# Kernel tuning notes

Measured on AMD Instinct MI355X. Metric: run time of the kernel, lower is better.

The kernel has to match this reference:

```python
import jax, jax.numpy as jnp
import numpy as np

B, S, D, H, O = 8, 4096, 512, 512, 512
NS, NC, SD = 4, 4, 8
CLIP, TEMP, SUP_SCALE, SUP_EPS, LN_EPS = 3.0, 1.0, 1.0, 1e-4, 1e-5


def _ln(x, w, b):
    m = jnp.mean(x, -1, keepdims=True)
    v = jnp.mean((x - m) ** 2, -1, keepdims=True)
    return (x - m) * jax.lax.rsqrt(v + LN_EPS) * w + b


def _lin(x, w, b):
    return x @ w.T + b


def setup_inputs() -> dict:
    key = jax.random.key(0)
    ks = iter(jax.random.split(key, 32))

    def W(shape):
        return 0.02 * jax.random.normal(next(ks), shape, jnp.float32)

    inp = {}
    inp['x'] = jax.random.normal(next(ks), (B, S, D), jnp.float32)
    inp['sb_norm_w'] = jnp.ones((D,), jnp.float32)
    inp['sb_norm_b'] = jnp.zeros((D,), jnp.float32)
    inp['sb_proj_w'] = W((NS, D)); inp['sb_proj_b'] = jnp.zeros((NS,), jnp.float32)
    inp['sb_sum_w'] = W((SD, 4)); inp['sb_sum_b'] = jnp.zeros((SD,), jnp.float32)
    inp['cb_norm_w'] = jnp.ones((D,), jnp.float32)
    inp['cb_norm_b'] = jnp.zeros((D,), jnp.float32)
    inp['cb_proj_w'] = W((NC, D)); inp['cb_proj_b'] = jnp.zeros((NC,), jnp.float32)
    inp['cb_sum_w'] = W((SD, 4)); inp['cb_sum_b'] = jnp.zeros((SD,), jnp.float32)
    inp['vn_norm_w'] = jnp.ones((D,), jnp.float32)
    inp['vn_norm_b'] = jnp.zeros((D,), jnp.float32)
    inp['vn_w1'] = W((H, D)); inp['vn_b1'] = jnp.zeros((H,), jnp.float32)
    inp['vn_w2'] = W((O, H)); inp['vn_b2'] = jnp.zeros((O,), jnp.float32)
    inp['un_norm_w'] = jnp.ones((D,), jnp.float32)
    inp['un_norm_b'] = jnp.zeros((D,), jnp.float32)
    inp['un_w1'] = W((H, D)); inp['un_b1'] = jnp.zeros((H,), jnp.float32)
    inp['un_w2'] = W((1, H)); inp['un_b2'] = jnp.zeros((1,), jnp.float32)
    inp['en_w'] = W((H, 1)); inp['en_b'] = jnp.zeros((H,), jnp.float32)
    inp['pr_w'] = W((H, 1)); inp['pr_b'] = jnp.zeros((H,), jnp.float32)
    inp['rs_w'] = W((H, 1)); inp['rs_b'] = jnp.zeros((H,), jnp.float32)
    inp['ssp_w'] = W((H, SD)); inp['ssp_b'] = jnp.zeros((H,), jnp.float32)
    inp['csp_w'] = W((H, SD)); inp['csp_b'] = jnp.zeros((H,), jnp.float32)
    inp['out_w'] = W((O, O + 5 * H)); inp['out_b'] = jnp.zeros((O,), jnp.float32)
    inp['support_logits'] = jnp.zeros((NS,), jnp.float32)
    inp['conflict_weights'] = jnp.ones((NC,), jnp.float32)
    inp['drive_bias'] = jnp.zeros((1,), jnp.float32)
    inp['bias_resistance'] = jnp.zeros((1,), jnp.float32)
    inp['update_threshold'] = jnp.ones((1,), jnp.float32)
    inp['eml_gamma'] = jnp.full((1,), 0.3, jnp.float32)
    inp['eml_lambda'] = jnp.ones((1,), jnp.float32)
    inp['eml_bias'] = jnp.zeros((1,), jnp.float32)
    return inp


def reference(x, sb_norm_w, sb_norm_b, sb_proj_w, sb_proj_b, sb_sum_w, sb_sum_b,
              cb_norm_w, cb_norm_b, cb_proj_w, cb_proj_b, cb_sum_w, cb_sum_b,
              vn_norm_w, vn_norm_b, vn_w1, vn_b1, vn_w2, vn_b2,
              un_norm_w, un_norm_b, un_w1, un_b1, un_w2, un_b2,
              en_w, en_b, pr_w, pr_b, rs_w, rs_b,
              ssp_w, ssp_b, csp_w, csp_b, out_w, out_b,
              support_logits, conflict_weights, drive_bias, bias_resistance,
              update_threshold, eml_gamma, eml_lambda, eml_bias):
    # Support bank: LN -> Linear -> softplus(+eps) -> stats -> summary Linear
    sf = jax.nn.softplus(_lin(_ln(x, sb_norm_w, sb_norm_b), sb_proj_w, sb_proj_b)) + SUP_EPS  # [B,S,NS]
    ls = jnp.log(sf)
    s_seed = jnp.concatenate([
        sf.mean(-1, keepdims=True), sf.std(-1, keepdims=True),
        ls.mean(-1, keepdims=True), ls.max(-1, keepdims=True)], -1)
    ss = _lin(s_seed, sb_sum_w, sb_sum_b)  # [B,S,SD]
    # Conflict bank
    cf = jax.nn.softplus(_lin(_ln(x, cb_norm_w, cb_norm_b), cb_proj_w, cb_proj_b))  # [B,S,NC]
    c_seed = jnp.concatenate([
        cf.mean(-1, keepdims=True), cf.std(-1, keepdims=True),
        cf.max(-1, keepdims=True), cf.min(-1, keepdims=True)], -1)
    cs = _lin(c_seed, cb_sum_w, cb_sum_b)  # [B,S,SD]
    # Drive / resistance
    sw = jax.nn.softmax(support_logits)
    drive = drive_bias + SUP_SCALE * (ls * sw).sum(-1, keepdims=True) / np.sqrt(NS)
    cw = jax.nn.softplus(conflict_weights)
    weighted_conflict = (cf * cw).sum(-1, keepdims=True) / np.sqrt(NC)
    u_h = jax.nn.gelu(_lin(_ln(x, un_norm_w, un_norm_b), un_w1, un_b1), approximate=False)
    uncertainty = jax.nn.softplus(_lin(u_h, un_w2, un_b2))  # [B,S,1]
    resistance = bias_resistance + weighted_conflict + uncertainty
    # EML unit (dim=1): bounded linear drive-resistance balance, warmup_eta=1.0
    e_raw = eml_gamma * drive - eml_lambda * resistance + eml_bias
    energy = CLIP * jnp.tanh(e_raw / CLIP)
    activation = jax.nn.sigmoid(energy / TEMP)
    precision = jax.nn.softplus(energy - update_threshold)
    # Value net
    v_h = jax.nn.gelu(_lin(_ln(x, vn_norm_w, vn_norm_b), vn_w1, vn_b1), approximate=False)
    value = _lin(v_h, vn_w2, vn_b2)  # [B,S,O]
    feats = jnp.concatenate([
        activation * value,
        _lin(energy, en_w, en_b),
        _lin(precision, pr_w, pr_b),
        _lin(resistance, rs_w, rs_b),
        _lin(ss, ssp_w, ssp_b),
        _lin(cs, csp_w, csp_b)], -1)  # [B,S,O+5H]
    return _lin(feats, out_w, out_b)  # [B,S,O]
```

## Files before the change

### kernel.cpp

```cpp
#include <hip/hip_runtime.h>
#include <stdint.h>

typedef unsigned short u16;
typedef __bf16 bf16x8 __attribute__((ext_vector_type(8)));
typedef float f32x4 __attribute__((ext_vector_type(4)));
typedef __attribute__((address_space(1))) void gvoid;
typedef __attribute__((address_space(3))) void lvoid;

#define NTOK 32768

__device__ __forceinline__ u16 f2bf(float f) {
    unsigned u = __float_as_uint(f);
    u += 0x7fffu + ((u >> 16) & 1u);
    return (u16)(u >> 16);
}
__device__ __forceinline__ float softplusf(float x) {
    return fmaxf(x, 0.f) + log1pf(expf(-fabsf(x)));
}
__device__ __forceinline__ float geluf(float x) {
    return 0.5f * x * (1.f + erff(x * 0.7071067811865475f));
}
__device__ __forceinline__ float wave_sum(float v) {
#pragma unroll
    for (int o = 32; o > 0; o >>= 1) v += __shfl_xor(v, o);
    return v;
}
__device__ __forceinline__ float blk_sum(float v) {
    __shared__ float sm[4];
    v = wave_sum(v);
    __syncthreads();
    if ((threadIdx.x & 63) == 0) sm[threadIdx.x >> 6] = v;
    __syncthreads();
    return sm[0] + sm[1] + sm[2] + sm[3];
}

__global__ void k_fold(
    const float* __restrict__ vnw1, const float* __restrict__ vnnw, const float* __restrict__ vnnb, const float* __restrict__ vnb1,
    const float* __restrict__ unw1, const float* __restrict__ unnw, const float* __restrict__ unnb, const float* __restrict__ unb1,
    const float* __restrict__ sbpw, const float* __restrict__ sbpb, const float* __restrict__ sbnw, const float* __restrict__ sbnb,
    const float* __restrict__ cbpw, const float* __restrict__ cbpb, const float* __restrict__ cbnw, const float* __restrict__ cbnb,
    const float* __restrict__ outw, const float* __restrict__ enw, const float* __restrict__ enb,
    const float* __restrict__ prw, const float* __restrict__ prb,
    const float* __restrict__ rsw, const float* __restrict__ rsb,
    const float* __restrict__ sspw, const float* __restrict__ sspb,
    const float* __restrict__ cspw, const float* __restrict__ cspb,
    const float* __restrict__ vnw2, const float* __restrict__ vnb2,
    u16* __restrict__ Astk, float* __restrict__ bstk, float* __restrict__ pb,
    u16* __restrict__ Aow, u16* __restrict__ vnT,
    float* __restrict__ a_en, float* __restrict__ a_pr, float* __restrict__ a_rs,
    float* __restrict__ b_vo, float* __restrict__ c_cn, float* __restrict__ Mss, float* __restrict__ Mcs)
{
    const int b = blockIdx.x, t = threadIdx.x;
    if (b < 1024) {
        const float *w1, *nw, *nb; float bias;
        if (b < 512) { w1 = vnw1 + (size_t)b * 512; nw = vnnw; nb = vnnb; bias = vnb1[b]; }
        else { int r = b - 512; w1 = unw1 + (size_t)r * 512; nw = unnw; nb = unnb; bias = unb1[r]; }
        float part = 0.f;
        for (int d = t; d < 512; d += 256) {
            float wv = w1[d];
            Astk[(size_t)b * 512 + d] = f2bf(wv * nw[d]);
            part += wv * nb[d];
        }
        float s = blk_sum(part);
        if (t == 0) bstk[b] = bias + s;
    } else if (b < 1032) {
        int j = b - 1024;
        const float *pw, *nw, *nb; float bias;
        if (j < 4) { pw = sbpw + j * 512; nw = sbnw; nb = sbnb; bias = sbpb[j]; }
        else { pw = cbpw + (j - 4) * 512; nw = cbnw; nb = cbnb; bias = cbpb[j - 4]; }
        float part = 0.f;
        for (int d = t; d < 512; d += 256) {
            float wv = pw[d];
            Astk[(size_t)(1024 + j) * 512 + d] = f2bf(wv * nw[d]);
            part += wv * nb[d];
        }
        float s = blk_sum(part);
        if (t == 0) pb[j] = bias + s;
    } else if (b < 1152) {
        for (int d = t; d < 512; d += 256) Astk[(size_t)b * 512 + d] = 0;
    } else if (b < 1664) {
        int i = b - 1152;
        const float* ow = outw + (size_t)i * 3072;
        float pen = 0, ppr = 0, prs = 0, pbv = 0, pcc = 0;
        float pms[8], pmc[8];
#pragma unroll
        for (int k = 0; k < 8; k++) { pms[k] = 0.f; pmc[k] = 0.f; }
        for (int h = t; h < 512; h += 256) {
            float o0 = ow[h];        Aow[(size_t)i * 512 + h] = f2bf(o0); pbv += o0 * vnb2[h];
            float o1 = ow[512 + h];  pen += o1 * enw[h]; pcc += o1 * enb[h];
            float o2 = ow[1024 + h]; ppr += o2 * prw[h]; pcc += o2 * prb[h];
            float o3 = ow[1536 + h]; prs += o3 * rsw[h]; pcc += o3 * rsb[h];
            float o4 = ow[2048 + h]; pcc += o4 * sspb[h];
            float o5 = ow[2560 + h]; pcc += o5 * cspb[h];
#pragma unroll
            for (int k = 0; k < 8; k++) { pms[k] += o4 * sspw[h * 8 + k]; pmc[k] += o5 * cspw[h * 8 + k]; }
        }
        float r;
        r = blk_sum(pen); if (t == 0) a_en[i] = r;
        r = blk_sum(ppr); if (t == 0) a_pr[i] = r;
        r = blk_sum(prs); if (t == 0) a_rs[i] = r;
        r = blk_sum(pbv); if (t == 0) b_vo[i] = r;
        r = blk_sum(pcc); if (t == 0) c_cn[i] = r;
        for (int k = 0; k < 8; k++) { r = blk_sum(pms[k]); if (t == 0) Mss[i * 8 + k] = r; }
        for (int k = 0; k < 8; k++) { r = blk_sum(pmc[k]); if (t == 0) Mcs[i * 8 + k] = r; }
    } else {
        int hrow = b - 1664;
        for (int o = t; o < 512; o += 256)
            vnT[(size_t)hrow * 512 + o] = f2bf(vnw2[(size_t)o * 512 + hrow]);
    }
}

__device__ __forceinline__ void gt_stage(const u16* __restrict__ A_, int lda,
                                         const u16* __restrict__ B_, int ldb, int kt,
                                         u16* dA, u16* dB, int w, int lrow, int lcol)
{
#pragma unroll
    for (int i = 0; i < 4; i++) {
        const int chunk = i * 4 + w;
        const int row = chunk * 8 + lrow;
        __builtin_amdgcn_global_load_lds((gvoid*)const_cast<u16*>(A_ + (size_t)row * lda + kt + lcol),
                                         (lvoid*)(dA + chunk * 512), 16, 0, 0);
        __builtin_amdgcn_global_load_lds((gvoid*)const_cast<u16*>(B_ + (size_t)row * ldb + kt + lcol),
                                         (lvoid*)(dB + chunk * 512), 16, 0, 0);
    }
}

__device__ __forceinline__ void gt_compute(const u16* lA, const u16* lB, f32x4 (&acc)[4][4],
                                           int wr, int wc, int frow, int fk, int sw)
{
#pragma unroll
    for (int ks = 0; ks < 2; ks++) {
        bf16x8 af[4], bfv[4];
        const int c = (ks * 32 + fk);
#pragma unroll
        for (int rt = 0; rt < 4; rt++)
            af[rt] = *(const bf16x8*)(lA + (wr + rt * 16 + frow) * 64 + (c ^ sw));
#pragma unroll
        for (int ct = 0; ct < 4; ct++)
            bfv[ct] = *(const bf16x8*)(lB + (wc + ct * 16 + frow) * 64 + (c ^ sw));
#pragma unroll
        for (int rt = 0; rt < 4; rt++)
#pragma unroll
            for (int ct = 0; ct < 4; ct++)
                acc[rt][ct] = __builtin_amdgcn_mfma_f32_16x16x32_bf16(af[rt], bfv[ct], acc[rt][ct], 0, 0, 0);
    }
}

__device__ __forceinline__ void gemm_tile(const u16* __restrict__ Ab, int lda,
                                          const u16* __restrict__ Bb, int ldb,
                                          int K, u16* sm, f32x4 (&acc)[4][4])
{
    const int t = threadIdx.x;
    const int w = t >> 6, l = t & 63;
    const int lrow = l >> 3;
    const int lcol = ((l ^ (((l >> 3) & 3) << 1)) & 7) * 8;
    const int wr = ((w >> 1) << 6), wc = ((w & 1) << 6);
    const int frow = l & 15, fk = ((l >> 4) << 3);
    const int sw = (frow & 3) << 4;
    u16* lA0 = sm;          u16* lA1 = sm + 8192;
    u16* lB0 = sm + 16384;  u16* lB1 = sm + 24576;

    gt_stage(Ab, lda, Bb, ldb, 0, lA0, lB0, w, lrow, lcol);
    __syncthreads();
    for (int kt = 0; kt < K; kt += 128) {
        if (kt + 64 < K) gt_stage(Ab, lda, Bb, ldb, kt + 64, lA1, lB1, w, lrow, lcol);
        gt_compute(lA0, lB0, acc, wr, wc, frow, fk, sw);
        __syncthreads();
        if (kt + 128 < K) gt_stage(Ab, lda, Bb, ldb, kt + 128, lA0, lB0, w, lrow, lcol);
        gt_compute(lA1, lB1, acc, wr, wc, frow, fk, sw);
        __syncthreads();
    }
}

__global__ __launch_bounds__(256, 2) void k_gemm_wvo(const u16* __restrict__ A, const u16* __restrict__ Bm,
                                                     u16* __restrict__ C)
{
    __shared__ __align__(16) u16 smem[32768];
    const f32x4 zero = {0.f, 0.f, 0.f, 0.f};
    f32x4 acc[4][4];
#pragma unroll
    for (int a = 0; a < 4; a++)
#pragma unroll
        for (int c = 0; c < 4; c++) acc[a][c] = zero;
    const u16* Ab = A + (size_t)blockIdx.y * 128 * 512;
    const u16* Bb = Bm + (size_t)blockIdx.x * 128 * 512;
    gemm_tile(Ab, 512, Bb, 512, 512, smem, acc);
    const int t = threadIdx.x, w = t >> 6, l = t & 63;
    const int rbase = blockIdx.y * 128 + ((w >> 1) << 6);
    const int cbase = blockIdx.x * 128 + ((w & 1) << 6);
    const int lr = ((l >> 4) << 2), lc = l & 15;
#pragma unroll
    for (int rt = 0; rt < 4; rt++)
#pragma unroll
        for (int ct = 0; ct < 4; ct++)
#pragma unroll
            for (int j = 0; j < 4; j++)
                C[(size_t)(rbase + rt * 16 + lr + j) * 512 + cbase + ct * 16 + lc] = f2bf(acc[rt][ct][j]);
}

__global__ void k_token(const float* __restrict__ x, u16* __restrict__ Ybf)
{
    const int w = threadIdx.x >> 6, l = threadIdx.x & 63;
    const int n = blockIdx.x * 4 + w;
    const float* xr = x + (size_t)n * 512;
    float4 xa = *(const float4*)(xr + 4 * l);
    float4 xb = *(const float4*)(xr + 256 + 4 * l);
    float v[8] = {xa.x, xa.y, xa.z, xa.w, xb.x, xb.y, xb.z, xb.w};
    float s1 = 0.f, s2 = 0.f;
#pragma unroll
    for (int c = 0; c < 8; c++) { s1 += v[c]; s2 += v[c] * v[c]; }
    s1 = wave_sum(s1); s2 = wave_sum(s2);
    const float mean = s1 * (1.f / 512.f);
    const float var = s2 * (1.f / 512.f) - mean * mean;
    const float rstd = rsqrtf(var + 1e-5f);
    float y[8];
#pragma unroll
    for (int c = 0; c < 8; c++) y[c] = (v[c] - mean) * rstd;
    *(ushort4*)(Ybf + (size_t)n * 512 + 4 * l) = make_ushort4(f2bf(y[0]), f2bf(y[1]), f2bf(y[2]), f2bf(y[3]));
    *(ushort4*)(Ybf + (size_t)n * 512 + 256 + 4 * l) = make_ushort4(f2bf(y[4]), f2bf(y[5]), f2bf(y[6]), f2bf(y[7]));
}

__global__ __launch_bounds__(256, 2) void k_gemm1(const u16* __restrict__ Y, const u16* __restrict__ Ast,
                                                  const float* __restrict__ bstk, const float* __restrict__ pb,
                                                  const float* __restrict__ unw2,
                                                  u16* __restrict__ H, float* __restrict__ wp,
                                                  float* __restrict__ wdotp)
{
    __shared__ __align__(16) u16 smem[32768];
    const f32x4 zero = {0.f, 0.f, 0.f, 0.f};
    f32x4 acc[4][4];
#pragma unroll
    for (int a = 0; a < 4; a++)
#pragma unroll
        for (int c = 0; c < 4; c++) acc[a][c] = zero;
    const int nwg = gridDim.x * gridDim.y;
    const int lin = blockIdx.y * gridDim.x + blockIdx.x;
    const int swz = (lin & 7) * (nwg >> 3) + (lin >> 3);
    const int by = swz / gridDim.x, bx = swz % gridDim.x;
    const u16* Ab = Y + (size_t)by * 128 * 512;
    const u16* Bb = Ast + (size_t)bx * 128 * 512;
    gemm_tile(Ab, 512, Bb, 512, 512, smem, acc);
    const int t = threadIdx.x, w = t >> 6, l = t & 63;
    const int wr = ((w >> 1) << 6), wc = ((w & 1) << 6);
    const int lr = ((l >> 4) << 2), lc = l & 15;
    if (bx == 8) {
        if ((w & 1) == 0 && lc < 8) {
            const float bv = pb[lc];
            const int rbase = by * 128 + wr;
#pragma unroll
            for (int rt = 0; rt < 4; rt++)
#pragma unroll
                for (int j = 0; j < 4; j++) {
                    const int n = rbase + rt * 16 + lr + j;
                    wp[(size_t)n * 8 + lc] = acc[rt][0][j] + bv;
                }
        }
        return;
    }
    if (bx >= 4) {
        const int cb = (bx - 4) * 128;
        float part[4][4];
#pragma unroll
        for (int rt = 0; rt < 4; rt++)
#pragma unroll
            for (int j = 0; j < 4; j++) part[rt][j] = 0.f;
#pragma unroll
        for (int ct = 0; ct < 4; ct++) {
            const int col = cb + wc + ct * 16 + lc;
            const float bv = bstk[512 + col];
            const float w2 = unw2[col];
#pragma unroll
            for (int rt = 0; rt < 4; rt++)
#pragma unroll
                for (int j = 0; j < 4; j++)
                    part[rt][j] += geluf(acc[rt][ct][j] + bv) * w2;
        }
        float* sf = (float*)smem;
        const int slot = ((w & 1) << 4) | lc;
        __syncthreads();
#pragma unroll
        for (int rt = 0; rt < 4; rt++)
#pragma unroll
            for (int j = 0; j < 4; j++)
                sf[(wr + rt * 16 + lr + j) * 32 + slot] = part[rt][j];
        __syncthreads();
        if (t < 128) {
            float s = 0.f;
#pragma unroll
            for (int k2 = 0; k2 < 32; k2++) s += sf[t * 32 + k2];
            wdotp[(size_t)(bx - 4) * NTOK + by * 128 + t] = s;
        }
        return;
    }
#pragma unroll
    for (int ct = 0; ct < 4; ct++) {
        const int col = wc + ct * 16 + lc;
        const float bv = bstk[bx * 128 + col];
#pragma unroll
        for (int rt = 0; rt < 4; rt++) {
            const int row = wr + rt * 16 + lr;
#pragma unroll
            for (int j = 0; j < 4; j++)
                smem[(row + j) * 136 + col] = f2bf(geluf(acc[rt][ct][j] + bv));
        }
    }
    __syncthreads();
    const size_t gbase = (size_t)(by * 128) * 512 + bx * 128;
#pragma unroll
    for (int jj = 0; jj < 8; jj++) {
        const int r = jj * 16 + (t >> 4), u = t & 15;
        bf16x8 vv = *(const bf16x8*)(smem + r * 136 + u * 8);
        *(bf16x8*)(H + gbase + (size_t)r * 512 + u * 8) = vv;
    }
}

__global__ void k_bank(const float* __restrict__ wp, const float* __restrict__ wdotp,
                       const float* __restrict__ unb2,
                       const float* __restrict__ sbsw, const float* __restrict__ sbsb,
                       const float* __restrict__ cbsw, const float* __restrict__ cbsb,
                       const float* __restrict__ suplog, const float* __restrict__ confw,
                       const float* __restrict__ drvb, const float* __restrict__ biasres,
                       const float* __restrict__ emlg, const float* __restrict__ emll,
                       const float* __restrict__ emlb, const float* __restrict__ updthr,
                       float* __restrict__ wss, float* __restrict__ wcs, float* __restrict__ wsc)
{
    const int n = blockIdx.x * 256 + threadIdx.x;
    float4 p0 = *(const float4*)(wp + (size_t)n * 8);
    float4 p1 = *(const float4*)(wp + (size_t)n * 8 + 4);
    float p[8] = {p0.x, p0.y, p0.z, p0.w, p1.x, p1.y, p1.z, p1.w};
    const float dot = wdotp[n] + wdotp[NTOK + n] + wdotp[2 * NTOK + n] + wdotp[3 * NTOK + n];
    float sf[4], lsv[4], cf[4];
#pragma unroll
    for (int j = 0; j < 4; j++) {
        sf[j] = softplusf(p[j]) + 1e-4f;
        lsv[j] = logf(sf[j]);
        cf[j] = softplusf(p[j + 4]);
    }
    const float smn = 0.25f * (sf[0] + sf[1] + sf[2] + sf[3]);
    float sd = 0.f;
#pragma unroll
    for (int j = 0; j < 4; j++) sd += (sf[j] - smn) * (sf[j] - smn);
    const float sstd = sqrtf(0.25f * sd);
    const float lmn = 0.25f * (lsv[0] + lsv[1] + lsv[2] + lsv[3]);
    const float lmx = fmaxf(fmaxf(lsv[0], lsv[1]), fmaxf(lsv[2], lsv[3]));
    const float cmn = 0.25f * (cf[0] + cf[1] + cf[2] + cf[3]);
    float cd = 0.f;
#pragma unroll
    for (int j = 0; j < 4; j++) cd += (cf[j] - cmn) * (cf[j] - cmn);
    const float cstd = sqrtf(0.25f * cd);
    const float cmx = fmaxf(fmaxf(cf[0], cf[1]), fmaxf(cf[2], cf[3]));
    const float cmi = fminf(fminf(cf[0], cf[1]), fminf(cf[2], cf[3]));
    float seed_s[4] = {smn, sstd, lmn, lmx};
    float seed_c[4] = {cmn, cstd, cmx, cmi};
    float a4[8], b4[8];
#pragma unroll
    for (int k = 0; k < 8; k++) {
        float a = sbsb[k], b2 = cbsb[k];
#pragma unroll
        for (int j = 0; j < 4; j++) { a += sbsw[k * 4 + j] * seed_s[j]; b2 += cbsw[k * 4 + j] * seed_c[j]; }
        a4[k] = a; b4[k] = b2;
    }
    *(float4*)(wss + (size_t)n * 8)     = make_float4(a4[0], a4[1], a4[2], a4[3]);
    *(float4*)(wss + (size_t)n * 8 + 4) = make_float4(a4[4], a4[5], a4[6], a4[7]);
    *(float4*)(wcs + (size_t)n * 8)     = make_float4(b4[0], b4[1], b4[2], b4[3]);
    *(float4*)(wcs + (size_t)n * 8 + 4) = make_float4(b4[4], b4[5], b4[6], b4[7]);
    float mx = fmaxf(fmaxf(suplog[0], suplog[1]), fmaxf(suplog[2], suplog[3]));
    float e[4], se = 0.f;
#pragma unroll
    for (int j = 0; j < 4; j++) { e[j] = expf(suplog[j] - mx); se += e[j]; }
    float dv = 0.f, wcv = 0.f;
#pragma unroll
    for (int j = 0; j < 4; j++) { dv += lsv[j] * (e[j] / se); wcv += cf[j] * softplusf(confw[j]); }
    const float drive = drvb[0] + 0.5f * dv;
    const float unc = softplusf(dot + unb2[0]);
    const float res = biasres[0] + 0.5f * wcv + unc;
    const float er = emlg[0] * drive - emll[0] * res + emlb[0];
    const float energy = 3.f * tanhf(er * (1.f / 3.f));
    const float act = 1.f / (1.f + expf(-energy));
    const float prc = softplusf(energy - updthr[0]);
    wsc[(size_t)n * 4 + 0] = act;
    wsc[(size_t)n * 4 + 1] = energy;
    wsc[(size_t)n * 4 + 2] = prc;
    wsc[(size_t)n * 4 + 3] = res;
}

__global__ __launch_bounds__(256, 2) void k_gemm2(const u16* __restrict__ H, const u16* __restrict__ Wvo,
    const float* __restrict__ wsc, const float* __restrict__ wss, const float* __restrict__ wcs,
    const float* __restrict__ a_en, const float* __restrict__ a_pr, const float* __restrict__ a_rs,
    const float* __restrict__ b_vo, const float* __restrict__ c_cn,
    const float* __restrict__ Mss, const float* __restrict__ Mcs,
    const float* __restrict__ outb, float* __restrict__ out)
{
    __shared__ __align__(16) u16 smem[32768];
    const f32x4 zero = {0.f, 0.f, 0.f, 0.f};
    f32x4 acc[4][4];
#pragma unroll
    for (int a = 0; a < 4; a++)
#pragma unroll
        for (int c = 0; c < 4; c++) acc[a][c] = zero;
    const int nwg = gridDim.x * gridDim.y;
    const int lin = blockIdx.y * gridDim.x + blockIdx.x;
    const int swz = (lin & 7) * (nwg >> 3) + (lin >> 3);
    const int by = swz / gridDim.x, bx = swz % gridDim.x;
    const u16* Ab = H + (size_t)by * 128 * 512;
    const u16* Bb = Wvo + (size_t)bx * 128 * 512;
    gemm_tile(Ab, 512, Bb, 512, 512, smem, acc);
    const int t = threadIdx.x, w = t >> 6, l = t & 63;
    const int rbase = by * 128 + ((w >> 1) << 6);
    const int cbase = bx * 128 + ((w & 1) << 6);
    const int lr = ((l >> 4) << 2), lc = l & 15;
    float bvo4[4], aen4[4], apr4[4], ars4[4], cc4[4], ms4[4][8], mc4[4][8];
#pragma unroll
    for (int ct = 0; ct < 4; ct++) {
        const int i = cbase + ct * 16 + lc;
        bvo4[ct] = b_vo[i]; aen4[ct] = a_en[i]; apr4[ct] = a_pr[i]; ars4[ct] = a_rs[i];
        cc4[ct] = c_cn[i] + outb[i];
#pragma unroll
        for (int k = 0; k < 8; k++) { ms4[ct][k] = Mss[i * 8 + k]; mc4[ct][k] = Mcs[i * 8 + k]; }
    }
#pragma unroll
    for (int rt = 0; rt < 4; rt++)
#pragma unroll
        for (int j = 0; j < 4; j++) {
            const int n = rbase + rt * 16 + lr + j;
            const float act = wsc[(size_t)n * 4 + 0];
            const float eng = wsc[(size_t)n * 4 + 1];
            const float prc = wsc[(size_t)n * 4 + 2];
            const float res = wsc[(size_t)n * 4 + 3];
            float sv[8], cv[8];
#pragma unroll
            for (int k = 0; k < 8; k++) { sv[k] = wss[(size_t)n * 8 + k]; cv[k] = wcs[(size_t)n * 8 + k]; }
#pragma unroll
            for (int ct = 0; ct < 4; ct++) {
                const int i = cbase + ct * 16 + lc;
                float o = act * (acc[rt][ct][j] + bvo4[ct]) + eng * aen4[ct] + prc * apr4[ct]
                        + res * ars4[ct] + cc4[ct];
#pragma unroll
                for (int k = 0; k < 8; k++) o += ms4[ct][k] * sv[k] + mc4[ct][k] * cv[k];
                out[(size_t)n * 512 + i] = o;
            }
        }
}

extern "C" void kernel_launch(void* const* d_in, const int* in_sizes, int n_in,
                              void* d_out, int out_size, void* d_ws, size_t ws_size,
                              hipStream_t stream)
{
    const float* x       = (const float*)d_in[0];
    const float* sbnw    = (const float*)d_in[1];
    const float* sbnb    = (const float*)d_in[2];
    const float* sbpw    = (const float*)d_in[3];
    const float* sbpb    = (const float*)d_in[4];
    const float* sbsw    = (const float*)d_in[5];
    const float* sbsb    = (const float*)d_in[6];
    const float* cbnw    = (const float*)d_in[7];
    const float* cbnb    = (const float*)d_in[8];
    const float* cbpw    = (const float*)d_in[9];
    const float* cbpb    = (const float*)d_in[10];
    const float* cbsw    = (const float*)d_in[11];
    const float* cbsb    = (const float*)d_in[12];
    const float* vnnw    = (const float*)d_in[13];
    const float* vnnb    = (const float*)d_in[14];
    const float* vnw1    = (const float*)d_in[15];
    const float* vnb1    = (const float*)d_in[16];
    const float* vnw2    = (const float*)d_in[17];
    const float* vnb2    = (const float*)d_in[18];
    const float* unnw    = (const float*)d_in[19];
    const float* unnb    = (const float*)d_in[20];
    const float* unw1    = (const float*)d_in[21];
    const float* unb1    = (const float*)d_in[22];
    const float* unw2    = (const float*)d_in[23];
    const float* unb2    = (const float*)d_in[24];
    const float* enw     = (const float*)d_in[25];
    const float* enb     = (const float*)d_in[26];
    const float* prw     = (const float*)d_in[27];
    const float* prb     = (const float*)d_in[28];
    const float* rsw     = (const float*)d_in[29];
    const float* rsb     = (const float*)d_in[30];
    const float* sspw    = (const float*)d_in[31];
    const float* sspb    = (const float*)d_in[32];
    const float* cspw    = (const float*)d_in[33];
    const float* cspb    = (const float*)d_in[34];
    const float* outw    = (const float*)d_in[35];
    const float* outb    = (const float*)d_in[36];
    const float* suplog  = (const float*)d_in[37];
    const float* confw   = (const float*)d_in[38];
    const float* drvb    = (const float*)d_in[39];
    const float* biasres = (const float*)d_in[40];
    const float* updthr  = (const float*)d_in[41];
    const float* emlg    = (const float*)d_in[42];
    const float* emll    = (const float*)d_in[43];
    const float* emlb    = (const float*)d_in[44];
    float* out = (float*)d_out;
    (void)in_sizes; (void)n_in; (void)out_size; (void)ws_size;

    char* wsp = (char*)d_ws;
    size_t off = 0;
    auto alloc = [&](size_t bytes) { char* p = wsp + off; off = (off + bytes + 255) & ~(size_t)255; return p; };
    u16*  Ybf  = (u16*)alloc((size_t)NTOK * 512 * 2);
    u16*  Hbf  = (u16*)alloc((size_t)NTOK * 512 * 2);
    u16*  Astk = (u16*)alloc(1152 * 512 * 2);
    float* bstk = (float*)alloc(1024 * 4);
    float* pb   = (float*)alloc(8 * 4);
    u16*  Aow  = (u16*)alloc(512 * 512 * 2);
    u16*  vnT  = (u16*)alloc(512 * 512 * 2);
    u16*  Wvo  = (u16*)alloc(512 * 512 * 2);
    float* a_en = (float*)alloc(512 * 4);
    float* a_pr = (float*)alloc(512 * 4);
    float* a_rs = (float*)alloc(512 * 4);
    float* b_vo = (float*)alloc(512 * 4);
    float* c_cn = (float*)alloc(512 * 4);
    float* Mss  = (float*)alloc(512 * 8 * 4);
    float* Mcs  = (float*)alloc(512 * 8 * 4);
    float* wp   = (float*)alloc((size_t)NTOK * 8 * 4);
    float* wdotp= (float*)alloc((size_t)NTOK * 4 * 4);
    float* wss  = (float*)alloc((size_t)NTOK * 8 * 4);
    float* wcs  = (float*)alloc((size_t)NTOK * 8 * 4);
    float* wsc  = (float*)alloc((size_t)NTOK * 4 * 4);

    k_fold<<<2176, 256, 0, stream>>>(vnw1, vnnw, vnnb, vnb1, unw1, unnw, unnb, unb1,
                                     sbpw, sbpb, sbnw, sbnb, cbpw, cbpb, cbnw, cbnb,
                                     outw, enw, enb, prw, prb, rsw, rsb, sspw, sspb, cspw, cspb,
                                     vnw2, vnb2,
                                     Astk, bstk, pb, Aow, vnT, a_en, a_pr, a_rs, b_vo, c_cn, Mss, Mcs);
    k_gemm_wvo<<<dim3(4, 4), 256, 0, stream>>>(Aow, vnT, Wvo);
    k_token<<<NTOK / 4, 256, 0, stream>>>(x, Ybf);
    k_gemm1<<<dim3(9, 256), 256, 0, stream>>>(Ybf, Astk, bstk, pb, unw2, Hbf, wp, wdotp);
    k_bank<<<NTOK / 256, 256, 0, stream>>>(wp, wdotp, unb2, sbsw, sbsb, cbsw, cbsb,
                                           suplog, confw, drvb, biasres, emlg, emll, emlb, updthr,
                                           wss, wcs, wsc);
    k_gemm2<<<dim3(4, 256), 256, 0, stream>>>(Hbf, Wvo, wsc, wss, wcs, a_en, a_pr, a_rs, b_vo, c_cn,
                                              Mss, Mcs, outb, out);
}
```

Before: 154.9 us.

## Load GEMM A operand directly into registers and fold Wvo GEMM into gemm1

The shared GEMM core now stages only the B tile through LDS (with an XOR swizzle) while each wave loads its A fragments straight from global memory into registers, halving LDS footprint and traffic. The small Wvo = Aow·vnT GEMM launch is removed and its 16 tiles run as an extra grid column (bx==9) of k_gemm1, saving a kernel launch. Launch bounds drop the min-2-blocks hint and shared memory shrinks. Direct uncoalesced-ish A loads may expose more global latency, and a __syncthreads was added before the epilogue reuse of smem.

```diff
diff --git a/kernel.cpp b/kernel.cpp
--- a/kernel.cpp
+++ b/kernel.cpp
@@ -110,92 +110,79 @@
     }
 }
 
-__device__ __forceinline__ void gt_stage(const u16* __restrict__ A_, int lda,
-                                         const u16* __restrict__ B_, int ldb, int kt,
-                                         u16* dA, u16* dB, int w, int lrow, int lcol)
-{
+__device__ __forceinline__ void stg_b(const u16* __restrict__ Bg, size_t brow0, int tile,
+                                      u16* lbase, int w, int l)
+{
+    const int kt = tile * 64;
+    const int rchunk = l >> 3;
+    const int gc = (((l & 7) ^ ((l >> 3) & 7)) << 3);
 #pragma unroll
     for (int i = 0; i < 4; i++) {
-        const int chunk = i * 4 + w;
-        const int row = chunk * 8 + lrow;
-        __builtin_amdgcn_global_load_lds((gvoid*)const_cast<u16*>(A_ + (size_t)row * lda + kt + lcol),
-                                         (lvoid*)(dA + chunk * 512), 16, 0, 0);
-        __builtin_amdgcn_global_load_lds((gvoid*)const_cast<u16*>(B_ + (size_t)row * ldb + kt + lcol),
-                                         (lvoid*)(dB + chunk * 512), 16, 0, 0);
-    }
-}
-
-__device__ __forceinline__ void gt_compute(const u16* lA, const u16* lB, f32x4 (&acc)[4][4],
-                                           int wr, int wc, int frow, int fk, int sw)
+        const int r0 = (w * 4 + i) * 8;
+        __builtin_amdgcn_global_load_lds(
+            (gvoid*)const_cast<u16*>(Bg + (brow0 + r0 + rchunk) * 512 + kt + gc),
+            (lvoid*)(lbase + r0 * 64), 16, 0, 0);
+    }
+}
+
+__device__ __forceinline__ void lda(const u16* __restrict__ Ag, size_t arow0, int tile,
+                                    bf16x8 (&ar)[4][2], int wr, int l)
+{
+    const int kt = tile * 64;
+    const int fkb = (l >> 4) << 3;
+#pragma unroll
+    for (int rt = 0; rt < 4; rt++)
+#pragma unroll
+        for (int ks = 0; ks < 2; ks++)
+            ar[rt][ks] = *(const bf16x8*)(Ag + (arow0 + wr + rt * 16 + (l & 15)) * 512 + kt + ks * 32 + fkb);
+}
+
+__device__ __forceinline__ void gcomp(const u16* lB, bf16x8 (&aw)[4][2], f32x4 (&acc)[4][4],
+                                      int wc, int l)
 {
 #pragma unroll
     for (int ks = 0; ks < 2; ks++) {
-        bf16x8 af[4], bfv[4];
-        const int c = (ks * 32 + fk);
+        bf16x8 bf[4];
+#pragma unroll
+        for (int ct = 0; ct < 4; ct++) {
+            const int row = wc + ct * 16 + (l & 15);
+            const int s = (ks * 4 + (l >> 4)) ^ (row & 7);
+            bf[ct] = *(const bf16x8*)(lB + row * 64 + (s << 3));
+        }
 #pragma unroll
         for (int rt = 0; rt < 4; rt++)
-            af[rt] = *(const bf16x8*)(lA + (wr + rt * 16 + frow) * 64 + (c ^ sw));
-#pragma unroll
-        for (int ct = 0; ct < 4; ct++)
-            bfv[ct] = *(const bf16x8*)(lB + (wc + ct * 16 + frow) * 64 + (c ^ sw));
-#pragma unroll
-        for (int rt = 0; rt < 4; rt++)
 #pragma unroll
             for (int ct = 0; ct < 4; ct++)
-                acc[rt][ct] = __builtin_amdgcn_mfma_f32_16x16x32_bf16(af[rt], bfv[ct], acc[rt][ct], 0, 0, 0);
-    }
-}
-
-__device__ __forceinline__ void gemm_tile(const u16* __restrict__ Ab, int lda,
-                                          const u16* __restrict__ Bb, int ldb,
-                                          int K, u16* sm, f32x4 (&acc)[4][4])
-{
-    const int t = threadIdx.x;
-    const int w = t >> 6, l = t & 63;
-    const int lrow = l >> 3;
-    const int lcol = ((l ^ (((l >> 3) & 3) << 1)) & 7) * 8;
+                acc[rt][ct] = __builtin_amdgcn_mfma_f32_16x16x32_bf16(aw[rt][ks], bf[ct], acc[rt][ct], 0, 0, 0);
+    }
+}
+
+__device__ __forceinline__ void gemm_areg(const u16* __restrict__ Ag, const u16* __restrict__ Bg,
+                                          size_t arow0, size_t brow0,
+                                          u16* sm, f32x4 (&acc)[4][4], int w, int l)
+{
     const int wr = ((w >> 1) << 6), wc = ((w & 1) << 6);
-    const int frow = l & 15, fk = ((l >> 4) << 3);
-    const int sw = (frow & 3) << 4;
-    u16* lA0 = sm;          u16* lA1 = sm + 8192;
-    u16* lB0 = sm + 16384;  u16* lB1 = sm + 24576;
-
-    gt_stage(Ab, lda, Bb, ldb, 0, lA0, lB0, w, lrow, lcol);
+    u16* const lB0 = sm;
+    u16* const lB1 = sm + 8192;
+    bf16x8 a0[4][2], a1[4][2];
+
+    stg_b(Bg, brow0, 0, lB0, w, l);
+    lda(Ag, arow0, 0, a0, wr, l);
     __syncthreads();
-    for (int kt = 0; kt < K; kt += 128) {
-        if (kt + 64 < K) gt_stage(Ab, lda, Bb, ldb, kt + 64, lA1, lB1, w, lrow, lcol);
-        gt_compute(lA0, lB0, acc, wr, wc, frow, fk, sw);
+#pragma unroll
+    for (int tp = 0; tp < 4; ++tp) {
+        const int t1 = 2 * tp + 1, t2 = 2 * tp + 2;
+        stg_b(Bg, brow0, t1, lB1, w, l);
+        lda(Ag, arow0, t1, a1, wr, l);
+        gcomp(lB0, a0, acc, wc, l);
         __syncthreads();
-        if (kt + 128 < K) gt_stage(Ab, lda, Bb, ldb, kt + 128, lA0, lB0, w, lrow, lcol);
-        gt_compute(lA1, lB1, acc, wr, wc, frow, fk, sw);
+        if (t2 < 8) {
+            stg_b(Bg, brow0, t2, lB0, w, l);
+            lda(Ag, arow0, t2, a0, wr, l);
+        }
+        gcomp(lB1, a1, acc, wc, l);
         __syncthreads();
     }
-}
-
-__global__ __launch_bounds__(256, 2) void k_gemm_wvo(const u16* __restrict__ A, const u16* __restrict__ Bm,
-                                                     u16* __restrict__ C)
-{
-    __shared__ __align__(16) u16 smem[32768];
-    const f32x4 zero = {0.f, 0.f, 0.f, 0.f};
-    f32x4 acc[4][4];
-#pragma unroll
-    for (int a = 0; a < 4; a++)
-#pragma unroll
-        for (int c = 0; c < 4; c++) acc[a][c] = zero;
-    const u16* Ab = A + (size_t)blockIdx.y * 128 * 512;
-    const u16* Bb = Bm + (size_t)blockIdx.x * 128 * 512;
-    gemm_tile(Ab, 512, Bb, 512, 512, smem, acc);
-    const int t = threadIdx.x, w = t >> 6, l = t & 63;
-    const int rbase = blockIdx.y * 128 + ((w >> 1) << 6);
-    const int cbase = blockIdx.x * 128 + ((w & 1) << 6);
-    const int lr = ((l >> 4) << 2), lc = l & 15;
-#pragma unroll
-    for (int rt = 0; rt < 4; rt++)
-#pragma unroll
-        for (int ct = 0; ct < 4; ct++)
-#pragma unroll
-            for (int j = 0; j < 4; j++)
-                C[(size_t)(rbase + rt * 16 + lr + j) * 512 + cbase + ct * 16 + lc] = f2bf(acc[rt][ct][j]);
 }
 
 __global__ void k_token(const float* __restrict__ x, u16* __restrict__ Ybf)
@@ -220,13 +207,15 @@
     *(ushort4*)(Ybf + (size_t)n * 512 + 256 + 4 * l) = make_ushort4(f2bf(y[4]), f2bf(y[5]), f2bf(y[6]), f2bf(y[7]));
 }
 
-__global__ __launch_bounds__(256, 2) void k_gemm1(const u16* __restrict__ Y, const u16* __restrict__ Ast,
-                                                  const float* __restrict__ bstk, const float* __restrict__ pb,
-                                                  const float* __restrict__ unw2,
-                                                  u16* __restrict__ H, float* __restrict__ wp,
-                                                  float* __restrict__ wdotp)
-{
-    __shared__ __align__(16) u16 smem[32768];
+__global__ __launch_bounds__(256) void k_gemm1(const u16* __restrict__ Y, const u16* __restrict__ Ast,
+                                               const float* __restrict__ bstk, const float* __restrict__ pb,
+                                               const float* __restrict__ unw2,
+                                               const u16* __restrict__ Aow, const u16* __restrict__ vnT,
+                                               u16* __restrict__ Wvo,
+                                               u16* __restrict__ H, float* __restrict__ wp,
+                                               float* __restrict__ wdotp)
+{
+    __shared__ __align__(16) u16 smem[18432];
     const f32x4 zero = {0.f, 0.f, 0.f, 0.f};
     f32x4 acc[4][4];
 #pragma unroll
@@ -237,12 +226,28 @@
     const int lin = blockIdx.y * gridDim.x + blockIdx.x;
     const int swz = (lin & 7) * (nwg >> 3) + (lin >> 3);
     const int by = swz / gridDim.x, bx = swz % gridDim.x;
-    const u16* Ab = Y + (size_t)by * 128 * 512;
-    const u16* Bb = Ast + (size_t)bx * 128 * 512;
-    gemm_tile(Ab, 512, Bb, 512, 512, smem, acc);
     const int t = threadIdx.x, w = t >> 6, l = t & 63;
     const int wr = ((w >> 1) << 6), wc = ((w & 1) << 6);
     const int lr = ((l >> 4) << 2), lc = l & 15;
+
+    if (bx == 9) {
+        if (by >= 16) return;
+        const size_t ar = (size_t)(by >> 2) * 128, br = (size_t)(by & 3) * 128;
+        gemm_areg(Aow, vnT, ar, br, smem, acc, w, l);
+        const int rbase = (by >> 2) * 128 + wr;
+        const int cbase = (by & 3) * 128 + wc;
+#pragma unroll
+        for (int rt = 0; rt < 4; rt++)
+#pragma unroll
+            for (int ct = 0; ct < 4; ct++)
+#pragma unroll
+                for (int j = 0; j < 4; j++)
+                    Wvo[(size_t)(rbase + rt * 16 + lr + j) * 512 + cbase + ct * 16 + lc] = f2bf(acc[rt][ct][j]);
+        return;
+    }
+
+    gemm_areg(Y, Ast, (size_t)by * 128, (size_t)bx * 128, smem, acc, w, l);
+
     if (bx == 8) {
         if ((w & 1) == 0 && lc < 8) {
             const float bv = pb[lc];
@@ -292,6 +297,7 @@
         }
         return;
     }
+    __syncthreads();
 #pragma unroll
     for (int ct = 0; ct < 4; ct++) {
         const int col = wc + ct * 16 + lc;
@@ -384,14 +390,14 @@
     wsc[(size_t)n * 4 + 3] = res;
 }
 
-__global__ __launch_bounds__(256, 2) void k_gemm2(const u16* __restrict__ H, const u16* __restrict__ Wvo,
+__global__ __launch_bounds__(256) void k_gemm2(const u16* __restrict__ H, const u16* __restrict__ Wvo,
     const float* __restrict__ wsc, const float* __restrict__ wss, const float* __restrict__ wcs,
     const float* __restrict__ a_en, const float* __restrict__ a_pr, const float* __restrict__ a_rs,
     const float* __restrict__ b_vo, const float* __restrict__ c_cn,
     const float* __restrict__ Mss, const float* __restrict__ Mcs,
     const float* __restrict__ outb, float* __restrict__ out)
 {
-    __shared__ __align__(16) u16 smem[32768];
+    __shared__ __align__(16) u16 smem[16384];
     const f32x4 zero = {0.f, 0.f, 0.f, 0.f};
     f32x4 acc[4][4];
 #pragma unroll
@@ -402,10 +408,10 @@
     const int lin = blockIdx.y * gridDim.x + blockIdx.x;
     const int swz = (lin & 7) * (nwg >> 3) + (lin >> 3);
     const int by = swz / gridDim.x, bx = swz % gridDim.x;
-    const u16* Ab = H + (size_t)by * 128 * 512;
-    const u16* Bb = Wvo + (size_t)bx * 128 * 512;
-    gemm_tile(Ab, 512, Bb, 512, 512, smem, acc);
     const int t = threadIdx.x, w = t >> 6, l = t & 63;
+
+    gemm_areg(H, Wvo, (size_t)by * 128, (size_t)bx * 128, smem, acc, w, l);
+
     const int rbase = by * 128 + ((w >> 1) << 6);
     const int cbase = bx * 128 + ((w & 1) << 6);
     const int lr = ((l >> 4) << 2), lc = l & 15;
@@ -523,9 +529,9 @@
                                      outw, enw, enb, prw, prb, rsw, rsb, sspw, sspb, cspw, cspb,
                                      vnw2, vnb2,
                                      Astk, bstk, pb, Aow, vnT, a_en, a_pr, a_rs, b_vo, c_cn, Mss, Mcs);
-    k_gemm_wvo<<<dim3(4, 4), 256, 0, stream>>>(Aow, vnT, Wvo);
     k_token<<<NTOK / 4, 256, 0, stream>>>(x, Ybf);
-    k_gemm1<<<dim3(9, 256), 256, 0, stream>>>(Ybf, Astk, bstk, pb, unw2, Hbf, wp, wdotp);
+    k_gemm1<<<dim3(10, 256), 256, 0, stream>>>(Ybf, Astk, bstk, pb, unw2, Aow, vnT, Wvo,
+                                               Hbf, wp, wdotp);
     k_bank<<<NTOK / 256, 256, 0, stream>>>(wp, wdotp, unb2, sbsw, sbsb, cbsw, cbsb,
                                            suplog, confw, drvb, biasres, emlg, emll, emlb, updthr,
                                            wss, wcs, wsc);
```

Result: slower. 271.4 us (+75.2%).
